# Performance work log

Hardware: AMD Instinct MI355X
Metric: run time of the kernel (lower is better)

## Reference

```python
import jax, jax.numpy as jnp
import numpy as np

B, NN, NC, H, V, K = 1024, 16, 16, 64, 100, 8
C = NN + NC
NEG = -1e9


def _ln_all(x, eps=1e-5):
    # torch.layer_norm(x, x.shape): normalize over ALL elements, no affine
    mu = x.mean()
    var = ((x - mu) ** 2).mean()
    return (x - mu) * jax.lax.rsqrt(var + eps)


def _ln_last(x, g, b, eps=1e-5):
    # nn.LayerNorm(H) with affine params
    mu = x.mean(-1, keepdims=True)
    var = ((x - mu) ** 2).mean(-1, keepdims=True)
    return (x - mu) * jax.lax.rsqrt(var + eps) * g + b


def _masked_ln(x, m, eps=1e-5):
    # x: [C,B,H], m: [C,B]; full-tensor layernorm over in-graph nodes only
    cnt = jnp.maximum(m.sum(1) * x.shape[-1], 1.0)
    mu = (x * m[..., None]).sum((1, 2)) / cnt
    d = x - mu[:, None, None]
    var = ((d * d) * m[..., None]).sum((1, 2)) / cnt
    return d * jax.lax.rsqrt(var + eps)[:, None, None]


def _forward(num_data, cat_data, num_w, num_b, cat_emb, fi_w1, fi_b1, fi_g, fi_be,
             fi_w2, fi_b2, gcn1_w, gcn1_b, gcn2_w, gcn2_b, pw1, pb1, pg, pbe, pw2, pb2):
    # numeric columns: Linear(1,H) per column == scalar * w + b
    fe_num = num_data[..., None] * num_w[None] + num_b[None]              # [B,NN,H]
    fe_num = _ln_all(jax.nn.relu(fe_num.reshape(B, NN * H)))
    fe_cat = cat_emb[jnp.arange(NC)[None, :], cat_data]                   # [B,NC,H]
    fe_cat = _ln_all(fe_cat.reshape(B, NC * H))
    feat = jnp.concatenate([fe_num, fe_cat], axis=1)                      # [B,C*H]
    fe3 = feat.reshape(B, C, H)
    # shared feature-importance MLP applied to every column slice (dropout = eval)
    h = _ln_last(jax.nn.relu(fe3 @ fi_w1 + fi_b1), fi_g, fi_be)
    imp = _ln_all((h @ fi_w2 + fi_b2)[..., 0])                            # [B,C]
    fe3 = fe3 * imp[..., None]
    feat = fe3.reshape(B, C * H)
    # top-K column selection per row + masked softmax
    _, idx = jax.lax.top_k(imp, K)                                        # [B,K]
    mask = jnp.zeros((B, C), jnp.float32).at[jnp.arange(B)[:, None], idx].set(1.0)
    p = jax.nn.softmax(jnp.where(mask > 0, imp, NEG), axis=1) * mask      # [B,C]
    # graph c: nodes = rows with column c in their top-K; zero column c,
    # adjacency = P P^T with zero diagonal, softmax over nonzero entries
    mT = mask.T                                                           # [C,B]
    pm = p[None, :, :] * mT[:, :, None] * (1.0 - jnp.eye(C))[:, None, :]  # [C,B,C]
    S = jnp.einsum('cik,cjk->cij', pm, pm)                                # [C,B,B]
    S = S * (1.0 - jnp.eye(B))
    pos = S > 0
    mx = jnp.max(jnp.where(pos, S, -jnp.inf), axis=(1, 2))
    mx = jnp.where(jnp.isfinite(mx), mx, 0.0)
    E = jnp.where(pos, jnp.exp(S - mx[:, None, None]), 0.0)
    Z = E.sum((1, 2))
    w = E / jnp.where(Z > 0, Z, 1.0)[:, None, None]
    # GCNConv normalization: add self-loops (weight 1) for in-graph nodes
    A = w + jnp.eye(B)[None] * mT[:, :, None]
    deg = A.sum(-1)
    dinv = jnp.where(deg > 0, jax.lax.rsqrt(deg), 0.0)
    An = dinv[:, :, None] * A * dinv[:, None, :]                          # [C,B,B]
    x = jnp.einsum('cij,jh->cih', An, feat @ gcn1_w) + gcn1_b
    x = _masked_ln(jax.nn.relu(x), mT)
    x = jnp.einsum('cij,cjh->cih', An, x @ gcn2_w) + gcn2_b
    x = _masked_ln(jax.nn.relu(x), mT)                                    # [C,B,H]
    # reassembly: each row gathers its K graph outputs, ordered by column id
    cols = jnp.sort(idx, axis=1)                                          # [B,K]
    gathered = x[cols, jnp.arange(B)[:, None]]                            # [B,K,H]
    full = jnp.concatenate([gathered, fe3], axis=1).reshape(B, (K + C) * H)
    return _ln_last(jax.nn.relu(full @ pw1 + pb1), pg, pbe) @ pw2 + pb2   # [B,2]


def setup_inputs() -> dict:
    key = jax.random.key(0)
    ks = jax.random.split(key, 12)
    s = 0.05
    f = jnp.float32
    return {
        'num_data': jax.random.normal(ks[0], (B, NN), f),
        'cat_data': jax.random.randint(ks[1], (B, NC), 0, V, jnp.int32),
        'num_w': jax.random.normal(ks[2], (NN, H), f) * s,
        'num_b': jnp.zeros((NN, H), f),
        'cat_emb': jax.random.normal(ks[3], (NC, V, H), f) * s,
        'fi_w1': jax.random.normal(ks[4], (H, H), f) * s,
        'fi_b1': jnp.zeros((H,), f),
        'fi_g': jnp.ones((H,), f),
        'fi_be': jnp.zeros((H,), f),
        'fi_w2': jax.random.normal(ks[5], (H, 1), f) * s,
        'fi_b2': jnp.zeros((1,), f),
        'gcn1_w': jax.random.normal(ks[6], (C * H, H), f) * s,
        'gcn1_b': jnp.zeros((H,), f),
        'gcn2_w': jax.random.normal(ks[7], (H, H), f) * s,
        'gcn2_b': jnp.zeros((H,), f),
        'pw1': jax.random.normal(ks[8], ((K + C) * H, H), f) * s,
        'pb1': jnp.zeros((H,), f),
        'pg': jnp.ones((H,), f),
        'pbe': jnp.zeros((H,), f),
        'pw2': jax.random.normal(ks[9], (H, 2), f) * s,
        'pb2': jnp.zeros((2,), f),
    }


def reference(num_data, cat_data, num_w, num_b, cat_emb, fi_w1, fi_b1, fi_g, fi_be,
              fi_w2, fi_b2, gcn1_w, gcn1_b, gcn2_w, gcn2_b, pw1, pb1, pg, pbe, pw2, pb2):
    return _forward(num_data, cat_data, num_w, num_b, cat_emb, fi_w1, fi_b1, fi_g, fi_be,
                    fi_w2, fi_b2, gcn1_w, gcn1_b, gcn2_w, gcn2_b, pw1, pb1, pg, pbe, pw2, pb2)
```

## Files before the change

kernel.cpp:

```cpp
#include <hip/hip_runtime.h>
#include <hip/hip_bf16.h>

#define BB   1024
#define NNUM 16
#define NCAT 16
#define HH   64
#define VV   100
#define KK   8
#define CC   32
#define CH   2048
#define FULLW 2560

#define OFF_FE3   0u
#define OFF_X1    2097152u
#define OFF_X2    4194304u
#define OFF_G     6291456u
#define OFF_SIMP  6356992u
#define OFF_P     6389760u
#define OFF_ROWE  6422528u
#define OFF_DINV  6455296u
#define OFF_F     6488064u
#define OFF_STATS 6520832u
#define OFF_Z     6520840u
#define OFF_X1S   6520872u
#define OFF_X2S   6520936u
#define OFF_COLS  6521000u
#define OFF_LIST  6529192u
#define OFF_CNT   6561960u
#define OFF_AOFF  6561992u
#define OFF_AN    6562048u

__device__ inline float wsum64(float v){
  #pragma unroll
  for (int o = 32; o; o >>= 1) v += __shfl_xor(v, o);
  return v;
}

__global__ __launch_bounds__(256) void k_init(float* ws){
  int t = threadIdx.x;
  if (t < 8)  ws[OFF_STATS + t] = 0.f;
  if (t < 64) ws[OFF_X1S + t] = 0.f;
  if (t < 64) ws[OFF_X2S + t] = 0.f;
  if (t < 32) ws[OFF_Z + t] = 0.f;
}

__global__ __launch_bounds__(256) void k_fe(const float* __restrict__ nd,
                                            const float* __restrict__ nw,
                                            const float* __restrict__ nb,
                                            const int* __restrict__ cd,
                                            const float* __restrict__ emb,
                                            float* __restrict__ ws){
  float* fe3 = ws + OFF_FE3;
  float lsn = 0.f, lssn = 0.f, lsc = 0.f, lssc = 0.f;
  int idx = blockIdx.x*256 + threadIdx.x;
  {
    int h4 = idx & 15, fn = (idx >> 4) & 15, b = (idx >> 8) & 1023;
    bool isNum = (idx < 262144);
    if (isNum){
      float s = nd[b*NNUM + fn];
      float4 w = *(const float4*)&nw[fn*HH + h4*4];
      float4 bi = *(const float4*)&nb[fn*HH + h4*4];
      float4 v;
      v.x = fmaxf(s*w.x + bi.x, 0.f);
      v.y = fmaxf(s*w.y + bi.y, 0.f);
      v.z = fmaxf(s*w.z + bi.z, 0.f);
      v.w = fmaxf(s*w.w + bi.w, 0.f);
      *(float4*)&fe3[b*CH + fn*HH + h4*4] = v;
      lsn = v.x+v.y+v.z+v.w;
      lssn = v.x*v.x+v.y*v.y+v.z*v.z+v.w*v.w;
    } else {
      int j = cd[b*NCAT + fn];
      float4 v = *(const float4*)&emb[((size_t)fn*VV + j)*HH + h4*4];
      *(float4*)&fe3[b*CH + (NNUM + fn)*HH + h4*4] = v;
      lsc = v.x+v.y+v.z+v.w;
      lssc = v.x*v.x+v.y*v.y+v.z*v.z+v.w*v.w;
    }
  }
  __shared__ float sh[16];
  lsn = wsum64(lsn); lssn = wsum64(lssn);
  lsc = wsum64(lsc); lssc = wsum64(lssc);
  int w = threadIdx.x >> 6;
  if ((threadIdx.x & 63) == 0){ sh[w] = lsn; sh[4+w] = lssn; sh[8+w] = lsc; sh[12+w] = lssc; }
  __syncthreads();
  if (threadIdx.x == 0){
    if (blockIdx.x < 1024){
      atomicAdd(ws + OFF_STATS + 0, sh[0]+sh[1]+sh[2]+sh[3]);
      atomicAdd(ws + OFF_STATS + 1, sh[4]+sh[5]+sh[6]+sh[7]);
    } else {
      atomicAdd(ws + OFF_STATS + 2, sh[8]+sh[9]+sh[10]+sh[11]);
      atomicAdd(ws + OFF_STATS + 3, sh[12]+sh[13]+sh[14]+sh[15]);
    }
  }
}

__global__ __launch_bounds__(256) void k_normfe(float* __restrict__ ws){
  const float Ninv = 1.f/1048576.f;
  int idx4 = blockIdx.x*256 + threadIdx.x;
  float* fe3 = ws + OFF_FE3;
  const float* st = ws + OFF_STATS;
  int c = (idx4 & 511) >> 4;
  float s, ssq;
  if (c < NNUM){ s = st[0]; ssq = st[1]; } else { s = st[2]; ssq = st[3]; }
  float mu = s*Ninv;
  float var = ssq*Ninv - mu*mu;
  float rs = rsqrtf(var + 1e-5f);
  float4 v = *(float4*)&fe3[idx4*4];
  v.x = (v.x - mu)*rs; v.y = (v.y - mu)*rs; v.z = (v.z - mu)*rs; v.w = (v.w - mu)*rs;
  *(float4*)&fe3[idx4*4] = v;
}

__global__ __launch_bounds__(256) void k_fi(const float* __restrict__ w1,
                                            const float* __restrict__ b1,
                                            const float* __restrict__ g,
                                            const float* __restrict__ be,
                                            const float* __restrict__ w2,
                                            const float* __restrict__ b2f,
                                            float* __restrict__ ws){
  __shared__ float w1s[64][65];
  __shared__ float xs[4][64];
  int wv = threadIdx.x >> 6, lane = threadIdx.x & 63;
  for (int q = threadIdx.x; q < 4096; q += 256) w1s[q >> 6][q & 63] = w1[q];
  __syncthreads();
  const float* fe3 = ws + OFF_FE3;
  float b1l = b1[lane], gl = g[lane], bel = be[lane], w2l = w2[lane], b2s = b2f[0];
  int gw = blockIdx.x*4 + wv;
  float ls = 0.f, lss = 0.f;
  for (int it = 0; it < 8; ++it){
    int row = gw + 4096*it;
    float x = fe3[(size_t)row*64 + lane];
    xs[wv][lane] = x;
    float t0 = 0.f, t1 = 0.f, t2 = 0.f, t3 = 0.f;
    #pragma unroll
    for (int k = 0; k < 64; k += 4){
      float4 xq = *(const float4*)&xs[wv][k];
      t0 += xq.x*w1s[k][lane];
      t1 += xq.y*w1s[k+1][lane];
      t2 += xq.z*w1s[k+2][lane];
      t3 += xq.w*w1s[k+3][lane];
    }
    float t = (t0+t1) + (t2+t3) + b1l;
    t = fmaxf(t, 0.f);
    float mu = wsum64(t)*(1.f/64.f);
    float d = t - mu;
    float var = wsum64(d*d)*(1.f/64.f);
    float rs = rsqrtf(var + 1e-5f);
    float h1 = d*rs*gl + bel;
    float s = wsum64(h1*w2l) + b2s;
    if (lane == 0) ws[OFF_SIMP + row] = s;
    ls += s; lss += s*s;
  }
  __shared__ float sh[8];
  if (lane == 0){ sh[wv] = ls; sh[4+wv] = lss; }
  __syncthreads();
  if (threadIdx.x == 0){
    atomicAdd(ws + OFF_STATS + 4, sh[0]+sh[1]+sh[2]+sh[3]);
    atomicAdd(ws + OFF_STATS + 5, sh[4]+sh[5]+sh[6]+sh[7]);
  }
}

__global__ __launch_bounds__(256) void k_topk(float* __restrict__ ws){
  int b = blockIdx.x;
  __shared__ float imp[CC];
  if (threadIdx.x < CC){
    const float Ninv = 1.f/32768.f;
    float s4 = ws[OFF_STATS+4], s5 = ws[OFF_STATS+5];
    float mu = s4*Ninv, var = s5*Ninv - mu*mu;
    float rs = rsqrtf(var + 1e-5f);
    imp[threadIdx.x] = (ws[OFF_SIMP + b*CC + threadIdx.x] - mu)*rs;
  }
  __syncthreads();
  if (threadIdx.x == 0){
    unsigned taken = 0;
    float m0 = 0.f;
    for (int t = 0; t < KK; t++){
      float best = -1e30f; int bi = 0;
      for (int c = 0; c < CC; c++){
        if (!((taken >> c) & 1u) && imp[c] > best){ best = imp[c]; bi = c; }
      }
      taken |= 1u << bi;
      if (t == 0) m0 = best;
    }
    float sum = 0.f;
    int* cols = (int*)(ws + OFF_COLS);
    int tn = 0;
    for (int c = 0; c < CC; c++){
      if ((taken >> c) & 1u){ cols[b*KK + tn] = c; tn++; sum += expf(imp[c] - m0); }
    }
    float inv = 1.f/sum;
    for (int c = 0; c < CC; c++){
      float pv = ((taken >> c) & 1u) ? expf(imp[c] - m0)*inv : 0.f;
      ws[OFF_P + b*CC + c] = pv;
    }
  }
  __syncthreads();
  float* fe3 = ws + OFF_FE3;
  for (int kq = threadIdx.x; kq < CH; kq += 256){
    fe3[b*CH + kq] *= imp[kq >> 6];
  }
}

__global__ __launch_bounds__(256) void k_lists(float* __restrict__ ws){
  int c = blockIdx.x;
  __shared__ int cnt_s;
  if (threadIdx.x == 0) cnt_s = 0;
  __syncthreads();
  int* list = (int*)(ws + OFF_LIST);
  for (int b = threadIdx.x; b < BB; b += 256){
    if (ws[OFF_P + b*CC + c] > 0.f){
      int slot = atomicAdd(&cnt_s, 1);
      list[c*BB + slot] = b;
    }
  }
  __syncthreads();
  if (threadIdx.x == 0) ((int*)(ws + OFF_CNT))[c] = cnt_s;
}

__global__ void k_offs(float* __restrict__ ws){
  if (threadIdx.x == 0){
    const int* cnt = (const int*)(ws + OFF_CNT);
    int* aoff = (int*)(ws + OFF_AOFF);
    int acc = 0;
    for (int c = 0; c < CC; c++){ aoff[c] = acc; acc += cnt[c]*cnt[c]; }
    aoff[CC] = acc;
  }
}

__global__ __launch_bounds__(256) void k_G(const float* __restrict__ w1g, float* __restrict__ ws){
  __shared__ float frow[4][CH];
  int wv = threadIdx.x >> 6, lane = threadIdx.x & 63;
  int b = blockIdx.x*4 + wv;
  const float* fe3 = ws + OFF_FE3;
  for (int q = 0; q < 32; q++) frow[wv][q*64 + lane] = fe3[b*CH + q*64 + lane];
  __syncthreads();
  float a0 = 0.f, a1 = 0.f, a2 = 0.f, a3 = 0.f;
  #pragma unroll 8
  for (int k = 0; k < CH; k += 4){
    float4 fq = *(const float4*)&frow[wv][k];
    a0 += fq.x*w1g[(k+0)*64 + lane];
    a1 += fq.y*w1g[(k+1)*64 + lane];
    a2 += fq.z*w1g[(k+2)*64 + lane];
    a3 += fq.w*w1g[(k+3)*64 + lane];
  }
  ws[OFF_G + b*64 + lane] = (a0+a1) + (a2+a3);
}

__global__ __launch_bounds__(256) void k_E(float* __restrict__ ws){
  int c = blockIdx.x;
  int n = ((const int*)(ws + OFF_CNT))[c];
  int r0 = blockIdx.y*32;
  if (r0 >= n) return;
  const int* list = (const int*)(ws + OFF_LIST) + c*BB;
  const float* p = ws + OFF_P;
  int base = ((const int*)(ws + OFF_AOFF))[c];
  float* An = ws + OFF_AN;
  __shared__ float pis[32][36];
  __shared__ float pT[32][72];
  int wv = threadIdx.x >> 6, lane = threadIdx.x & 63;
  for (int idx = threadIdx.x; idx < 1024; idx += 256){
    int r = idx >> 5, u = idx & 31;
    int ii = r0 + r;
    float v = 0.f;
    if (ii < n && u != c) v = p[list[ii]*CC + u];
    pis[r][u] = v;
  }
  float re[8] = {0.f,0.f,0.f,0.f,0.f,0.f,0.f,0.f};
  int rowBase = r0 + wv*8;
  for (int jt = 0; jt < n; jt += 64){
    __syncthreads();
    for (int idx = threadIdx.x; idx < 2048; idx += 256){
      int t = idx & 63, u = idx >> 6;
      int jj = jt + t;
      float v = 0.f;
      if (jj < n) v = p[list[jj]*CC + u];
      pT[u][t] = v;
    }
    __syncthreads();
    int jj = jt + lane;
    bool jok = (jj < n);
    #pragma unroll
    for (int r = 0; r < 8; r++){
      int row = rowBase + r;
      if (row < n){
        float4 pi0 = *(const float4*)&pis[wv*8 + r][0];
        float4 pi1 = *(const float4*)&pis[wv*8 + r][4];
        float4 pi2 = *(const float4*)&pis[wv*8 + r][8];
        float4 pi3 = *(const float4*)&pis[wv*8 + r][12];
        float4 pi4 = *(const float4*)&pis[wv*8 + r][16];
        float4 pi5 = *(const float4*)&pis[wv*8 + r][20];
        float4 pi6 = *(const float4*)&pis[wv*8 + r][24];
        float4 pi7 = *(const float4*)&pis[wv*8 + r][28];
        float s0 = pi0.x*pT[0][lane]  + pi1.x*pT[4][lane]  + pi2.x*pT[8][lane]  + pi3.x*pT[12][lane]
                 + pi4.x*pT[16][lane] + pi5.x*pT[20][lane] + pi6.x*pT[24][lane] + pi7.x*pT[28][lane];
        float s1 = pi0.y*pT[1][lane]  + pi1.y*pT[5][lane]  + pi2.y*pT[9][lane]  + pi3.y*pT[13][lane]
                 + pi4.y*pT[17][lane] + pi5.y*pT[21][lane] + pi6.y*pT[25][lane] + pi7.y*pT[29][lane];
        float s2 = pi0.z*pT[2][lane]  + pi1.z*pT[6][lane]  + pi2.z*pT[10][lane] + pi3.z*pT[14][lane]
                 + pi4.z*pT[18][lane] + pi5.z*pT[22][lane] + pi6.z*pT[26][lane] + pi7.z*pT[30][lane];
        float s3 = pi0.w*pT[3][lane]  + pi1.w*pT[7][lane]  + pi2.w*pT[11][lane] + pi3.w*pT[15][lane]
                 + pi4.w*pT[19][lane] + pi5.w*pT[23][lane] + pi6.w*pT[27][lane] + pi7.w*pT[31][lane];
        float S = (s0+s1) + (s2+s3);
        float Ev = 0.f;
        if (jok && jj != row && S > 0.f) Ev = __expf(S);
        if (jok) An[(size_t)base + (size_t)row*n + jj] = Ev;
        re[r] += Ev;
      }
    }
  }
  float zpart = 0.f;
  #pragma unroll
  for (int r = 0; r < 8; r++){
    float rsum = wsum64(re[r]);
    int row = rowBase + r;
    if (lane == 0 && row < n){
      ws[OFF_ROWE + c*BB + row] = rsum;
      zpart += rsum;
    }
  }
  __shared__ float sh[4];
  if (lane == 0) sh[wv] = zpart;
  __syncthreads();
  if (threadIdx.x == 0) atomicAdd(ws + OFF_Z + c, sh[0]+sh[1]+sh[2]+sh[3]);
}

__global__ __launch_bounds__(256) void k_scl(float* __restrict__ ws){
  int c = blockIdx.x;
  int n = ((const int*)(ws + OFF_CNT))[c];
  int ii = blockIdx.y*256 + threadIdx.x;
  if (ii >= n) return;
  float z = ws[OFF_Z + c];
  float zp = (z > 0.f) ? z : 1.f;
  float re = ws[OFF_ROWE + c*BB + ii];
  float di = rsqrtf(re/zp + 1.0f);
  ws[OFF_DINV + c*BB + ii] = di;
  ws[OFF_F    + c*BB + ii] = di*rsqrtf(zp);
}

__global__ __launch_bounds__(256) void k_agg(const float* __restrict__ src, int chanStride,
                                             const float* __restrict__ bias,
                                             float* __restrict__ outb,
                                             float* __restrict__ statsb,
                                             float* __restrict__ ws){
  int c = blockIdx.x;
  int n = ((const int*)(ws + OFF_CNT))[c];
  int r0 = blockIdx.y*16;
  if (r0 >= n) return;
  int base = ((const int*)(ws + OFF_AOFF))[c];
  const int* lst = (const int*)(ws + OFF_LIST) + c*BB;
  const float* E = ws + OFF_AN + (size_t)base;
  const float* fpos = ws + OFF_F + c*BB;
  const float* dpos = ws + OFF_DINV + c*BB;
  const float* srcc = src + (size_t)c*(size_t)chanStride*64;
  __shared__ float cf[16][128];
  __shared__ float sl[128][64];
  __shared__ float frow_s[16];
  int wv = threadIdx.x >> 6, lane = threadIdx.x & 63;
  if (threadIdx.x < 16){
    int rr = r0 + threadIdx.x;
    frow_s[threadIdx.x] = (rr < n) ? fpos[rr] : 0.f;
  }
  int rw = wv*4;
  float acc[4] = {0.f,0.f,0.f,0.f};
  for (int jt = 0; jt < n; jt += 128){
    __syncthreads();
    #pragma unroll
    for (int s = 0; s < 8; s++){
      int slot = threadIdx.x + s*256;
      int j = slot >> 4, q = slot & 15;
      int jj = jt + j;
      float4 v = make_float4(0.f,0.f,0.f,0.f);
      if (jj < n){
        int jg = lst[jj];
        v = *(const float4*)&srcc[(size_t)jg*64 + q*4];
      }
      *(float4*)&sl[j][q*4] = v;
    }
    #pragma unroll
    for (int s = 0; s < 8; s++){
      int idx = threadIdx.x + s*256;
      int r = idx >> 7, j = idx & 127;
      int row = r0 + r, jj = jt + j;
      float v = 0.f;
      if (row < n && jj < n){
        if (jj == row){ float d = dpos[row]; v = d*d; }
        else v = E[(size_t)row*n + jj] * fpos[jj] * frow_s[r];
      }
      cf[r][j] = v;
    }
    __syncthreads();
    int jcnt = n - jt; if (jcnt > 128) jcnt = 128;
    int jcnt4 = (jcnt + 3) & ~3;
    for (int j = 0; j < jcnt4; j += 4){
      float v0 = sl[j+0][lane];
      float v1 = sl[j+1][lane];
      float v2 = sl[j+2][lane];
      float v3 = sl[j+3][lane];
      #pragma unroll
      for (int r = 0; r < 4; r++){
        float4 c4 = *(const float4*)&cf[rw + r][j];
        acc[r] += c4.x*v0 + c4.y*v1 + c4.z*v2 + c4.w*v3;
      }
    }
  }
  float bl = bias[lane];
  float s = 0.f, ssq = 0.f;
  #pragma unroll
  for (int r = 0; r < 4; r++){
    int row = r0 + rw + r;
    if (row < n){
      float a = fmaxf(acc[r] + bl, 0.f);
      outb[((size_t)c*BB + lst[row])*64 + lane] = a;
      s += a; ssq += a*a;
    }
  }
  s = wsum64(s); ssq = wsum64(ssq);
  __shared__ float shs[4], shq[4];
  if (lane == 0){ shs[wv] = s; shq[wv] = ssq; }
  __syncthreads();
  if (threadIdx.x == 0){
    float ts = shs[0]+shs[1]+shs[2]+shs[3];
    float tq = shq[0]+shq[1]+shq[2]+shq[3];
    if (tq != 0.f){
      atomicAdd(statsb + 2*c,     ts);
      atomicAdd(statsb + 2*c + 1, tq);
    }
  }
}

__global__ __launch_bounds__(256) void k_y(const float* __restrict__ w2g, float* __restrict__ ws){
  __shared__ float w2s[64][65];
  __shared__ float xs[4][64];
  int wv = threadIdx.x >> 6, lane = threadIdx.x & 63;
  for (int q = threadIdx.x; q < 4096; q += 256) w2s[q >> 6][q & 63] = w2g[q];
  __syncthreads();
  int c = blockIdx.x;
  int n = ((const int*)(ws + OFF_CNT))[c];
  const int* list = (const int*)(ws + OFF_LIST);
  float* x1 = ws + OFF_X1;
  float cntf = fmaxf((float)(n*64), 1.f);
  float mu = ws[OFF_X1S + 2*c]/cntf;
  float var = ws[OFF_X1S + 2*c + 1]/cntf - mu*mu;
  float rs = rsqrtf(var + 1e-5f);
  for (int ii = blockIdx.y*4 + wv; ii < n; ii += 64){
    int i = list[c*BB + ii];
    size_t bse = ((size_t)c*BB + i)*64;
    float xn = (x1[bse + lane] - mu)*rs;
    xs[wv][lane] = xn;
    float y0 = 0.f, y1 = 0.f, y2 = 0.f, y3 = 0.f;
    #pragma unroll
    for (int k = 0; k < 64; k += 4){
      float4 xq = *(const float4*)&xs[wv][k];
      y0 += xq.x*w2s[k][lane];
      y1 += xq.y*w2s[k+1][lane];
      y2 += xq.z*w2s[k+2][lane];
      y3 += xq.w*w2s[k+3][lane];
    }
    x1[bse + lane] = (y0+y1) + (y2+y3);
  }
}

__global__ __launch_bounds__(256) void k_final(const float* __restrict__ pw1,
                                               const float* __restrict__ pb1,
                                               const float* __restrict__ pg,
                                               const float* __restrict__ pbe,
                                               const float* __restrict__ pw2,
                                               const float* __restrict__ pb2,
                                               float* __restrict__ ws,
                                               float* __restrict__ out){
  __shared__ float fr[4][FULLW];
  int wv = threadIdx.x >> 6, lane = threadIdx.x & 63;
  int b = blockIdx.x*4 + wv;
  const int* cols = (const int*)(ws + OFF_COLS);
  const int* cnt  = (const int*)(ws + OFF_CNT);
  const float* x2 = ws + OFF_X2;
  const float* fe3 = ws + OFF_FE3;
  #pragma unroll
  for (int t = 0; t < KK; t++){
    int ct = cols[b*KK + t];
    float cf = fmaxf((float)(cnt[ct]*64), 1.f);
    float mu = ws[OFF_X2S + 2*ct]/cf;
    float var = ws[OFF_X2S + 2*ct + 1]/cf - mu*mu;
    float rs = rsqrtf(var + 1e-5f);
    fr[wv][t*64 + lane] = (x2[((size_t)ct*BB + b)*64 + lane] - mu)*rs;
  }
  #pragma unroll
  for (int q = 0; q < 32; q++) fr[wv][512 + q*64 + lane] = fe3[b*CH + q*64 + lane];
  __syncthreads();
  float a0 = 0.f, a1 = 0.f, a2 = 0.f, a3 = 0.f;
  #pragma unroll 8
  for (int k = 0; k < FULLW; k += 4){
    float4 fq = *(const float4*)&fr[wv][k];
    a0 += fq.x*pw1[(k+0)*64 + lane];
    a1 += fq.y*pw1[(k+1)*64 + lane];
    a2 += fq.z*pw1[(k+2)*64 + lane];
    a3 += fq.w*pw1[(k+3)*64 + lane];
  }
  float acc = (a0+a1) + (a2+a3) + pb1[lane];
  acc = fmaxf(acc, 0.f);
  float mu = wsum64(acc)*(1.f/64.f);
  float d = acc - mu;
  float var = wsum64(d*d)*(1.f/64.f);
  float rs = rsqrtf(var + 1e-5f);
  float zn = d*rs*pg[lane] + pbe[lane];
  float s0 = wsum64(zn*pw2[lane*2 + 0]);
  float s1 = wsum64(zn*pw2[lane*2 + 1]);
  if (lane == 0){
    out[b*2 + 0] = s0 + pb2[0];
    out[b*2 + 1] = s1 + pb2[1];
  }
}

extern "C" void kernel_launch(void* const* d_in, const int* in_sizes, int n_in,
                              void* d_out, int out_size, void* d_ws, size_t ws_size,
                              hipStream_t stream){
  (void)in_sizes; (void)n_in; (void)out_size; (void)ws_size;
  const float* num_data = (const float*)d_in[0];
  const int*   cat_data = (const int*)d_in[1];
  const float* num_w   = (const float*)d_in[2];
  const float* num_b   = (const float*)d_in[3];
  const float* cat_emb = (const float*)d_in[4];
  const float* fi_w1   = (const float*)d_in[5];
  const float* fi_b1   = (const float*)d_in[6];
  const float* fi_g    = (const float*)d_in[7];
  const float* fi_be   = (const float*)d_in[8];
  const float* fi_w2   = (const float*)d_in[9];
  const float* fi_b2   = (const float*)d_in[10];
  const float* gcn1_w  = (const float*)d_in[11];
  const float* gcn1_b  = (const float*)d_in[12];
  const float* gcn2_w  = (const float*)d_in[13];
  const float* gcn2_b  = (const float*)d_in[14];
  const float* pw1     = (const float*)d_in[15];
  const float* pb1     = (const float*)d_in[16];
  const float* pg      = (const float*)d_in[17];
  const float* pbe     = (const float*)d_in[18];
  const float* pw2     = (const float*)d_in[19];
  const float* pb2     = (const float*)d_in[20];
  float* ws  = (float*)d_ws;
  float* out = (float*)d_out;

  k_init<<<1, 256, 0, stream>>>(ws);
  k_fe<<<2048, 256, 0, stream>>>(num_data, num_w, num_b, cat_data, cat_emb, ws);
  k_normfe<<<2048, 256, 0, stream>>>(ws);
  k_fi<<<1024, 256, 0, stream>>>(fi_w1, fi_b1, fi_g, fi_be, fi_w2, fi_b2, ws);
  k_topk<<<1024, 256, 0, stream>>>(ws);
  k_lists<<<32, 256, 0, stream>>>(ws);
  k_offs<<<1, 64, 0, stream>>>(ws);
  k_G<<<256, 256, 0, stream>>>(gcn1_w, ws);
  k_E<<<dim3(32, 32), 256, 0, stream>>>(ws);
  k_scl<<<dim3(32, 4), 256, 0, stream>>>(ws);
  k_agg<<<dim3(32, 64), 256, 0, stream>>>(ws + OFF_G, 0, gcn1_b, ws + OFF_X1, ws + OFF_X1S, ws);
  k_y<<<dim3(32, 16), 256, 0, stream>>>(gcn2_w, ws);
  k_agg<<<dim3(32, 64), 256, 0, stream>>>(ws + OFF_X1, BB, gcn2_b, ws + OFF_X2, ws + OFF_X2S, ws);
  k_final<<<256, 256, 0, stream>>>(pw1, pb1, pg, pbe, pw2, pb2, ws, out);
}
```

Measured before the change: 535.2 us.

## Recompute adjacency exponentials in aggregation instead of materializing dense per-graph matrix

Stops writing the dense exp(P P^T) adjacency matrix to global memory in the row-sum kernel and drops the offset-prefix kernel. Each aggregation kernel now recomputes the adjacency entries on the fly from the P rows held in shared memory, tiled 64 columns at a time. This removes a large global write and two re-reads of roughly sum n_c^2 floats, plus one launch. In exchange the 32-term dot products and exps are computed three times, and the aggregation tile shrinks from 128 to 64 columns.

After: 644.8 us. +20.5%, slower.

```diff
diff --git a/kernel.cpp b/kernel.cpp
--- a/kernel.cpp
+++ b/kernel.cpp
@@ -27,8 +27,6 @@
 #define OFF_COLS  6521000u
 #define OFF_LIST  6529192u
 #define OFF_CNT   6561960u
-#define OFF_AOFF  6561992u
-#define OFF_AN    6562048u
 
 __device__ inline float wsum64(float v){
   #pragma unroll
@@ -215,16 +213,6 @@
   if (threadIdx.x == 0) ((int*)(ws + OFF_CNT))[c] = cnt_s;
 }
 
-__global__ void k_offs(float* __restrict__ ws){
-  if (threadIdx.x == 0){
-    const int* cnt = (const int*)(ws + OFF_CNT);
-    int* aoff = (int*)(ws + OFF_AOFF);
-    int acc = 0;
-    for (int c = 0; c < CC; c++){ aoff[c] = acc; acc += cnt[c]*cnt[c]; }
-    aoff[CC] = acc;
-  }
-}
-
 __global__ __launch_bounds__(256) void k_G(const float* __restrict__ w1g, float* __restrict__ ws){
   __shared__ float frow[4][CH];
   int wv = threadIdx.x >> 6, lane = threadIdx.x & 63;
@@ -244,15 +232,13 @@
   ws[OFF_G + b*64 + lane] = (a0+a1) + (a2+a3);
 }
 
-__global__ __launch_bounds__(256) void k_E(float* __restrict__ ws){
+__global__ __launch_bounds__(256) void k_rowE(float* __restrict__ ws){
   int c = blockIdx.x;
   int n = ((const int*)(ws + OFF_CNT))[c];
   int r0 = blockIdx.y*32;
   if (r0 >= n) return;
   const int* list = (const int*)(ws + OFF_LIST) + c*BB;
   const float* p = ws + OFF_P;
-  int base = ((const int*)(ws + OFF_AOFF))[c];
-  float* An = ws + OFF_AN;
   __shared__ float pis[32][36];
   __shared__ float pT[32][72];
   int wv = threadIdx.x >> 6, lane = threadIdx.x & 63;
@@ -298,10 +284,7 @@
         float s3 = pi0.w*pT[3][lane]  + pi1.w*pT[7][lane]  + pi2.w*pT[11][lane] + pi3.w*pT[15][lane]
                  + pi4.w*pT[19][lane] + pi5.w*pT[23][lane] + pi6.w*pT[27][lane] + pi7.w*pT[31][lane];
         float S = (s0+s1) + (s2+s3);
-        float Ev = 0.f;
-        if (jok && jj != row && S > 0.f) Ev = __expf(S);
-        if (jok) An[(size_t)base + (size_t)row*n + jj] = Ev;
-        re[r] += Ev;
+        if (jok && jj != row && S > 0.f) re[r] += __expf(S);
       }
     }
   }
@@ -343,26 +326,43 @@
   int n = ((const int*)(ws + OFF_CNT))[c];
   int r0 = blockIdx.y*16;
   if (r0 >= n) return;
-  int base = ((const int*)(ws + OFF_AOFF))[c];
   const int* lst = (const int*)(ws + OFF_LIST) + c*BB;
-  const float* E = ws + OFF_AN + (size_t)base;
+  const float* p = ws + OFF_P;
   const float* fpos = ws + OFF_F + c*BB;
   const float* dpos = ws + OFF_DINV + c*BB;
   const float* srcc = src + (size_t)c*(size_t)chanStride*64;
-  __shared__ float cf[16][128];
-  __shared__ float sl[128][64];
+  __shared__ float pis[16][36];
+  __shared__ float pT[32][72];
+  __shared__ float sl[64][64];
+  __shared__ float cf[16][68];
   __shared__ float frow_s[16];
   int wv = threadIdx.x >> 6, lane = threadIdx.x & 63;
   if (threadIdx.x < 16){
     int rr = r0 + threadIdx.x;
     frow_s[threadIdx.x] = (rr < n) ? fpos[rr] : 0.f;
   }
+  for (int idx = threadIdx.x; idx < 512; idx += 256){
+    int r = idx >> 5, u = idx & 31;
+    int ii = r0 + r;
+    float v = 0.f;
+    if (ii < n && u != c) v = p[lst[ii]*CC + u];
+    pis[r][u] = v;
+  }
   int rw = wv*4;
   float acc[4] = {0.f,0.f,0.f,0.f};
-  for (int jt = 0; jt < n; jt += 128){
+  for (int jt = 0; jt < n; jt += 64){
     __syncthreads();
     #pragma unroll
     for (int s = 0; s < 8; s++){
+      int idx = threadIdx.x + s*256;
+      int t = idx & 63, u = idx >> 6;
+      int jj = jt + t;
+      float v = 0.f;
+      if (jj < n) v = p[lst[jj]*CC + u];
+      pT[u][t] = v;
+    }
+    #pragma unroll
+    for (int s = 0; s < 4; s++){
       int slot = threadIdx.x + s*256;
       int j = slot >> 4, q = slot & 15;
       int jj = jt + j;
@@ -373,22 +373,41 @@
       }
       *(float4*)&sl[j][q*4] = v;
     }
+    __syncthreads();
+    int jj = jt + lane;
+    bool jok = (jj < n);
+    float fj = jok ? fpos[jj] : 0.f;
     #pragma unroll
-    for (int s = 0; s < 8; s++){
-      int idx = threadIdx.x + s*256;
-      int r = idx >> 7, j = idx & 127;
-      int row = r0 + r, jj = jt + j;
+    for (int r = 0; r < 4; r++){
+      int row = r0 + rw + r;
       float v = 0.f;
-      if (row < n && jj < n){
-        if (jj == row){ float d = dpos[row]; v = d*d; }
-        else v = E[(size_t)row*n + jj] * fpos[jj] * frow_s[r];
+      if (row < n && jok){
+        if (jj == row){
+          float d = dpos[row]; v = d*d;
+        } else {
+          float4 pi0 = *(const float4*)&pis[rw+r][0];
+          float4 pi1 = *(const float4*)&pis[rw+r][4];
+          float4 pi2 = *(const float4*)&pis[rw+r][8];
+          float4 pi3 = *(const float4*)&pis[rw+r][12];
+          float4 pi4 = *(const float4*)&pis[rw+r][16];
+          float4 pi5 = *(const float4*)&pis[rw+r][20];
+          float4 pi6 = *(const float4*)&pis[rw+r][24];
+          float4 pi7 = *(const float4*)&pis[rw+r][28];
+          float s0 = pi0.x*pT[0][lane]  + pi1.x*pT[4][lane]  + pi2.x*pT[8][lane]  + pi3.x*pT[12][lane]
+                   + pi4.x*pT[16][lane] + pi5.x*pT[20][lane] + pi6.x*pT[24][lane] + pi7.x*pT[28][lane];
+          float s1 = pi0.y*pT[1][lane]  + pi1.y*pT[5][lane]  + pi2.y*pT[9][lane]  + pi3.y*pT[13][lane]
+                   + pi4.y*pT[17][lane] + pi5.y*pT[21][lane] + pi6.y*pT[25][lane] + pi7.y*pT[29][lane];
+          float s2 = pi0.z*pT[2][lane]  + pi1.z*pT[6][lane]  + pi2.z*pT[10][lane] + pi3.z*pT[14][lane]
+                   + pi4.z*pT[18][lane] + pi5.z*pT[22][lane] + pi6.z*pT[26][lane] + pi7.z*pT[30][lane];
+          float s3 = pi0.w*pT[3][lane]  + pi1.w*pT[7][lane]  + pi2.w*pT[11][lane] + pi3.w*pT[15][lane]
+                   + pi4.w*pT[19][lane] + pi5.w*pT[23][lane] + pi6.w*pT[27][lane] + pi7.w*pT[31][lane];
+          float S = (s0+s1) + (s2+s3);
+          if (S > 0.f) v = __expf(S)*fj*frow_s[rw+r];
+        }
       }
-      cf[r][j] = v;
-    }
-    __syncthreads();
-    int jcnt = n - jt; if (jcnt > 128) jcnt = 128;
-    int jcnt4 = (jcnt + 3) & ~3;
-    for (int j = 0; j < jcnt4; j += 4){
+      cf[rw+r][lane] = v;
+    }
+    for (int j = 0; j < 64; j += 4){
       float v0 = sl[j+0][lane];
       float v1 = sl[j+1][lane];
       float v2 = sl[j+2][lane];
@@ -475,9 +494,9 @@
   #pragma unroll
   for (int t = 0; t < KK; t++){
     int ct = cols[b*KK + t];
-    float cf = fmaxf((float)(cnt[ct]*64), 1.f);
-    float mu = ws[OFF_X2S + 2*ct]/cf;
-    float var = ws[OFF_X2S + 2*ct + 1]/cf - mu*mu;
+    float cfv = fmaxf((float)(cnt[ct]*64), 1.f);
+    float mu = ws[OFF_X2S + 2*ct]/cfv;
+    float var = ws[OFF_X2S + 2*ct + 1]/cfv - mu*mu;
     float rs = rsqrtf(var + 1e-5f);
     fr[wv][t*64 + lane] = (x2[((size_t)ct*BB + b)*64 + lane] - mu)*rs;
   }
@@ -542,9 +561,8 @@
   k_fi<<<1024, 256, 0, stream>>>(fi_w1, fi_b1, fi_g, fi_be, fi_w2, fi_b2, ws);
   k_topk<<<1024, 256, 0, stream>>>(ws);
   k_lists<<<32, 256, 0, stream>>>(ws);
-  k_offs<<<1, 64, 0, stream>>>(ws);
   k_G<<<256, 256, 0, stream>>>(gcn1_w, ws);
-  k_E<<<dim3(32, 32), 256, 0, stream>>>(ws);
+  k_rowE<<<dim3(32, 32), 256, 0, stream>>>(ws);
   k_scl<<<dim3(32, 4), 256, 0, stream>>>(ws);
   k_agg<<<dim3(32, 64), 256, 0, stream>>>(ws + OFF_G, 0, gcn1_b, ws + OFF_X1, ws + OFF_X1S, ws);
   k_y<<<dim3(32, 16), 256, 0, stream>>>(gcn2_w, ws);
```

## Fold feature layernorm into k_fi/k_topk and tile G/final GEMMs over rows

Applied to the files above, without the earlier changes.

Removes the separate k_normfe pass: the per-group layernorm is now applied on the fly when k_fi reads fe3, and k_topk applies it together with the importance scaling when it writes fe3 back. k_G and k_final are restructured so each block handles 16 rows and each wave handles 4 rows, staging 512-wide chunks in shared memory and reusing each weight load across the 4 rows. This cuts global weight traffic and one full read/write pass over fe3. In exchange the GEMM kernels launch only 64 blocks, which lowers occupancy and may leave many CUs idle.

Result: slower. 796.7 us (+48.9%).

```diff
diff --git a/kernel.cpp b/kernel.cpp
--- a/kernel.cpp
+++ b/kernel.cpp
@@ -93,22 +93,6 @@
   }
 }
 
-__global__ __launch_bounds__(256) void k_normfe(float* __restrict__ ws){
-  const float Ninv = 1.f/1048576.f;
-  int idx4 = blockIdx.x*256 + threadIdx.x;
-  float* fe3 = ws + OFF_FE3;
-  const float* st = ws + OFF_STATS;
-  int c = (idx4 & 511) >> 4;
-  float s, ssq;
-  if (c < NNUM){ s = st[0]; ssq = st[1]; } else { s = st[2]; ssq = st[3]; }
-  float mu = s*Ninv;
-  float var = ssq*Ninv - mu*mu;
-  float rs = rsqrtf(var + 1e-5f);
-  float4 v = *(float4*)&fe3[idx4*4];
-  v.x = (v.x - mu)*rs; v.y = (v.y - mu)*rs; v.z = (v.z - mu)*rs; v.w = (v.w - mu)*rs;
-  *(float4*)&fe3[idx4*4] = v;
-}
-
 __global__ __launch_bounds__(256) void k_fi(const float* __restrict__ w1,
                                             const float* __restrict__ b1,
                                             const float* __restrict__ g,
@@ -122,12 +106,20 @@
   for (int q = threadIdx.x; q < 4096; q += 256) w1s[q >> 6][q & 63] = w1[q];
   __syncthreads();
   const float* fe3 = ws + OFF_FE3;
+  const float* st = ws + OFF_STATS;
+  const float NinvG = 1.f/1048576.f;
+  float mun = st[0]*NinvG, varn = st[1]*NinvG - mun*mun;
+  float rsn = rsqrtf(varn + 1e-5f);
+  float muc = st[2]*NinvG, varc = st[3]*NinvG - muc*muc;
+  float rsc = rsqrtf(varc + 1e-5f);
   float b1l = b1[lane], gl = g[lane], bel = be[lane], w2l = w2[lane], b2s = b2f[0];
   int gw = blockIdx.x*4 + wv;
   float ls = 0.f, lss = 0.f;
   for (int it = 0; it < 8; ++it){
     int row = gw + 4096*it;
-    float x = fe3[(size_t)row*64 + lane];
+    bool isn = (row & 31) < NNUM;
+    float mu0 = isn ? mun : muc, rs0 = isn ? rsn : rsc;
+    float x = (fe3[(size_t)row*64 + lane] - mu0)*rs0;
     xs[wv][lane] = x;
     float t0 = 0.f, t1 = 0.f, t2 = 0.f, t3 = 0.f;
     #pragma unroll
@@ -194,8 +186,21 @@
   }
   __syncthreads();
   float* fe3 = ws + OFF_FE3;
-  for (int kq = threadIdx.x; kq < CH; kq += 256){
-    fe3[b*CH + kq] *= imp[kq >> 6];
+  const float* st = ws + OFF_STATS;
+  const float NinvG = 1.f/1048576.f;
+  float mun = st[0]*NinvG, varn = st[1]*NinvG - mun*mun;
+  float rsn = rsqrtf(varn + 1e-5f);
+  float muc = st[2]*NinvG, varc = st[3]*NinvG - muc*muc;
+  float rsc = rsqrtf(varc + 1e-5f);
+  for (int q4 = threadIdx.x; q4 < 512; q4 += 256){
+    int c = q4 >> 4;
+    float mu, rs;
+    if (c < NNUM){ mu = mun; rs = rsn; } else { mu = muc; rs = rsc; }
+    float im = imp[c]*rs;
+    float4 v = *(float4*)&fe3[b*CH + q4*4];
+    v.x = (v.x - mu)*im; v.y = (v.y - mu)*im;
+    v.z = (v.z - mu)*im; v.w = (v.w - mu)*im;
+    *(float4*)&fe3[b*CH + q4*4] = v;
   }
 }
 
@@ -226,22 +231,37 @@
 }
 
 __global__ __launch_bounds__(256) void k_G(const float* __restrict__ w1g, float* __restrict__ ws){
-  __shared__ float frow[4][CH];
+  __shared__ float rs_[16][516];
   int wv = threadIdx.x >> 6, lane = threadIdx.x & 63;
-  int b = blockIdx.x*4 + wv;
+  int b0 = blockIdx.x*16;
   const float* fe3 = ws + OFF_FE3;
-  for (int q = 0; q < 32; q++) frow[wv][q*64 + lane] = fe3[b*CH + q*64 + lane];
-  __syncthreads();
-  float a0 = 0.f, a1 = 0.f, a2 = 0.f, a3 = 0.f;
-  #pragma unroll 8
-  for (int k = 0; k < CH; k += 4){
-    float4 fq = *(const float4*)&frow[wv][k];
-    a0 += fq.x*w1g[(k+0)*64 + lane];
-    a1 += fq.y*w1g[(k+1)*64 + lane];
-    a2 += fq.z*w1g[(k+2)*64 + lane];
-    a3 += fq.w*w1g[(k+3)*64 + lane];
-  }
-  ws[OFF_G + b*64 + lane] = (a0+a1) + (a2+a3);
+  float acc[4] = {0.f,0.f,0.f,0.f};
+  for (int kc = 0; kc < CH; kc += 512){
+    __syncthreads();
+    #pragma unroll
+    for (int s = 0; s < 8; s++){
+      int slot = threadIdx.x + s*256;
+      int r = slot >> 7, q = slot & 127;
+      float4 v = *(const float4*)&fe3[(size_t)(b0 + r)*CH + kc + q*4];
+      *(float4*)&rs_[r][q*4] = v;
+    }
+    __syncthreads();
+    int rbase = wv*4;
+    for (int k = 0; k < 512; k += 4){
+      float wa = w1g[(size_t)(kc+k+0)*64 + lane];
+      float wb = w1g[(size_t)(kc+k+1)*64 + lane];
+      float wc = w1g[(size_t)(kc+k+2)*64 + lane];
+      float wd = w1g[(size_t)(kc+k+3)*64 + lane];
+      #pragma unroll
+      for (int r = 0; r < 4; r++){
+        float4 f = *(const float4*)&rs_[rbase + r][k];
+        acc[r] += f.x*wa + f.y*wb + f.z*wc + f.w*wd;
+      }
+    }
+  }
+  #pragma unroll
+  for (int r = 0; r < 4; r++)
+    ws[OFF_G + (size_t)(b0 + wv*4 + r)*64 + lane] = acc[r];
 }
 
 __global__ __launch_bounds__(256) void k_E(float* __restrict__ ws){
@@ -465,46 +485,83 @@
                                                const float* __restrict__ pb2,
                                                float* __restrict__ ws,
                                                float* __restrict__ out){
-  __shared__ float fr[4][FULLW];
+  __shared__ float ck[16][516];
+  __shared__ float nf[CC][2];
+  __shared__ int cols_s[16][8];
   int wv = threadIdx.x >> 6, lane = threadIdx.x & 63;
-  int b = blockIdx.x*4 + wv;
+  int b0 = blockIdx.x*16;
   const int* cols = (const int*)(ws + OFF_COLS);
   const int* cnt  = (const int*)(ws + OFF_CNT);
   const float* x2 = ws + OFF_X2;
   const float* fe3 = ws + OFF_FE3;
-  #pragma unroll
-  for (int t = 0; t < KK; t++){
-    int ct = cols[b*KK + t];
+  if (threadIdx.x < 32){
+    int ct = threadIdx.x;
     float cf = fmaxf((float)(cnt[ct]*64), 1.f);
     float mu = ws[OFF_X2S + 2*ct]/cf;
     float var = ws[OFF_X2S + 2*ct + 1]/cf - mu*mu;
+    nf[ct][0] = mu; nf[ct][1] = rsqrtf(var + 1e-5f);
+  }
+  if (threadIdx.x < 128){
+    int r = threadIdx.x >> 3, t = threadIdx.x & 7;
+    cols_s[r][t] = cols[(b0 + r)*KK + t];
+  }
+  float acc[4] = {0.f,0.f,0.f,0.f};
+  for (int kc = 0; kc < FULLW; kc += 512){
+    __syncthreads();
+    if (kc == 0){
+      #pragma unroll
+      for (int s = 0; s < 8; s++){
+        int slot = threadIdx.x + s*256;
+        int r = slot >> 7, q = slot & 127;
+        int t = q >> 4, h4 = q & 15;
+        int ct = cols_s[r][t];
+        float mu = nf[ct][0], rsv = nf[ct][1];
+        float4 v = *(const float4*)&x2[((size_t)ct*BB + b0 + r)*64 + h4*4];
+        v.x = (v.x - mu)*rsv; v.y = (v.y - mu)*rsv;
+        v.z = (v.z - mu)*rsv; v.w = (v.w - mu)*rsv;
+        *(float4*)&ck[r][q*4] = v;
+      }
+    } else {
+      #pragma unroll
+      for (int s = 0; s < 8; s++){
+        int slot = threadIdx.x + s*256;
+        int r = slot >> 7, q = slot & 127;
+        float4 v = *(const float4*)&fe3[(size_t)(b0 + r)*CH + (kc - 512) + q*4];
+        *(float4*)&ck[r][q*4] = v;
+      }
+    }
+    __syncthreads();
+    int rbase = wv*4;
+    for (int k = 0; k < 512; k += 4){
+      float wa = pw1[(size_t)(kc+k+0)*64 + lane];
+      float wb = pw1[(size_t)(kc+k+1)*64 + lane];
+      float wc = pw1[(size_t)(kc+k+2)*64 + lane];
+      float wd = pw1[(size_t)(kc+k+3)*64 + lane];
+      #pragma unroll
+      for (int r = 0; r < 4; r++){
+        float4 f = *(const float4*)&ck[rbase + r][k];
+        acc[r] += f.x*wa + f.y*wb + f.z*wc + f.w*wd;
+      }
+    }
+  }
+  float bl = pb1[lane], gl = pg[lane], bel = pbe[lane];
+  float w20 = pw2[lane*2 + 0], w21 = pw2[lane*2 + 1];
+  float o0 = pb2[0], o1 = pb2[1];
+  #pragma unroll
+  for (int r = 0; r < 4; r++){
+    int b = b0 + wv*4 + r;
+    float a = fmaxf(acc[r] + bl, 0.f);
+    float mu = wsum64(a)*(1.f/64.f);
+    float d = a - mu;
+    float var = wsum64(d*d)*(1.f/64.f);
     float rs = rsqrtf(var + 1e-5f);
-    fr[wv][t*64 + lane] = (x2[((size_t)ct*BB + b)*64 + lane] - mu)*rs;
-  }
-  #pragma unroll
-  for (int q = 0; q < 32; q++) fr[wv][512 + q*64 + lane] = fe3[b*CH + q*64 + lane];
-  __syncthreads();
-  float a0 = 0.f, a1 = 0.f, a2 = 0.f, a3 = 0.f;
-  #pragma unroll 8
-  for (int k = 0; k < FULLW; k += 4){
-    float4 fq = *(const float4*)&fr[wv][k];
-    a0 += fq.x*pw1[(k+0)*64 + lane];
-    a1 += fq.y*pw1[(k+1)*64 + lane];
-    a2 += fq.z*pw1[(k+2)*64 + lane];
-    a3 += fq.w*pw1[(k+3)*64 + lane];
-  }
-  float acc = (a0+a1) + (a2+a3) + pb1[lane];
-  acc = fmaxf(acc, 0.f);
-  float mu = wsum64(acc)*(1.f/64.f);
-  float d = acc - mu;
-  float var = wsum64(d*d)*(1.f/64.f);
-  float rs = rsqrtf(var + 1e-5f);
-  float zn = d*rs*pg[lane] + pbe[lane];
-  float s0 = wsum64(zn*pw2[lane*2 + 0]);
-  float s1 = wsum64(zn*pw2[lane*2 + 1]);
-  if (lane == 0){
-    out[b*2 + 0] = s0 + pb2[0];
-    out[b*2 + 1] = s1 + pb2[1];
+    float zn = d*rs*gl + bel;
+    float s0 = wsum64(zn*w20);
+    float s1 = wsum64(zn*w21);
+    if (lane == 0){
+      out[b*2 + 0] = s0 + o0;
+      out[b*2 + 1] = s1 + o1;
+    }
   }
 }
 
@@ -538,16 +595,15 @@
 
   k_init<<<1, 256, 0, stream>>>(ws);
   k_fe<<<2048, 256, 0, stream>>>(num_data, num_w, num_b, cat_data, cat_emb, ws);
-  k_normfe<<<2048, 256, 0, stream>>>(ws);
   k_fi<<<1024, 256, 0, stream>>>(fi_w1, fi_b1, fi_g, fi_be, fi_w2, fi_b2, ws);
   k_topk<<<1024, 256, 0, stream>>>(ws);
   k_lists<<<32, 256, 0, stream>>>(ws);
   k_offs<<<1, 64, 0, stream>>>(ws);
-  k_G<<<256, 256, 0, stream>>>(gcn1_w, ws);
+  k_G<<<64, 256, 0, stream>>>(gcn1_w, ws);
   k_E<<<dim3(32, 32), 256, 0, stream>>>(ws);
   k_scl<<<dim3(32, 4), 256, 0, stream>>>(ws);
   k_agg<<<dim3(32, 64), 256, 0, stream>>>(ws + OFF_G, 0, gcn1_b, ws + OFF_X1, ws + OFF_X1S, ws);
   k_y<<<dim3(32, 16), 256, 0, stream>>>(gcn2_w, ws);
   k_agg<<<dim3(32, 64), 256, 0, stream>>>(ws + OFF_X1, BB, gcn2_b, ws + OFF_X2, ws + OFF_X2S, ws);
-  k_final<<<256, 256, 0, stream>>>(pw1, pb1, pg, pbe, pw2, pb2, ws, out);
-}
+  k_final<<<64, 256, 0, stream>>>(pw1, pb1, pg, pbe, pw2, pb2, ws, out);
+}
```
